# Performance work log

Hardware: AMD Instinct MI355X
Metric: run time of the kernel (lower is better)

The kernel has to match this reference:

```python
import jax, jax.numpy as jnp
import numpy as np

EMBED_DIM = 512
NUM_HEADS = 8
N_WIRES = 8  # kernel uses only first N_WIRES dims of each head vector


def setup_inputs() -> dict:
    key = jax.random.key(0)
    x = jax.random.normal(key, (8, 1024, EMBED_DIM), dtype=jnp.float32)
    return {"x": x}


def reference(x):
    B, S, E = x.shape
    H = NUM_HEADS
    dk = E // H
    # [B, H, S, dk]
    xh = x.reshape(B, S, H, dk).transpose(0, 2, 1, 3)
    # Quantum RY-overlap kernel closed form:
    #   RY(-y) RY(x) |0> = RY(x - y) |0>  =>  <0...0|psi> = prod_w cos((x_w - y_w)/2)
    # Only the first N_WIRES components of each head vector are used
    # (states.view(-1)[0] reads the first batch row's |0..0> amplitude).
    xw = xh[..., :N_WIRES]  # [B, H, S, NW]
    scores = jnp.ones((B, H, S, S), dtype=x.dtype)
    for w in range(N_WIRES):  # fixed small loop, fuses under jit
        diff = xw[:, :, :, None, w] - xw[:, :, None, :, w]  # [B, H, S, S]
        scores = scores * jnp.cos(diff * 0.5)
    scores = jnp.abs(scores)
    attn = jax.nn.softmax(scores, axis=-1)  # dropout is identity at eval
    out = jnp.einsum("bhij,bhjd->bhid", attn, xh)  # [B, H, S, dk]
    return out.transpose(0, 2, 1, 3).reshape(B, S, E)
```

## Files before the change

kernel.cpp:

```cpp
#include <hip/hip_runtime.h>

#define B_  8
#define S_  1024
#define E_  512
#define TI  64
#define TJ  64

typedef _Float16 half_t;
typedef _Float16 half2_t __attribute__((ext_vector_type(2)));
typedef _Float16 half8_t __attribute__((ext_vector_type(8)));
typedef float    floatx16 __attribute__((ext_vector_type(16)));
typedef unsigned int uint2v __attribute__((ext_vector_type(2)));
typedef unsigned int uint4v __attribute__((ext_vector_type(4)));

#define PHI_BYTES ((size_t)64 * S_ * 32 * 2)
#define VT_BYTES  ((size_t)64 * 64 * S_ * 2)

#define GLOAD_LDS16(g, l)                                                        \
    __builtin_amdgcn_global_load_lds((const __attribute__((address_space(1))) void*)(g), \
                                     (__attribute__((address_space(3))) void*)(l), 16, 0, 0)

__global__ __launch_bounds__(256) void precompute_kernel(const float* __restrict__ x,
                                                         half_t* __restrict__ phi,
                                                         half_t* __restrict__ vt) {
    const int bh  = blockIdx.y;
    const int b   = bh >> 3, h = bh & 7;
    const int jb0 = blockIdx.x * 128;
    const int t   = threadIdx.x;
    __shared__ half_t tsh[128 * 65];

    {
        const int jj = t >> 1, sel = t & 1;
        const int j  = jb0 + jj;
        const float* px = x + (size_t)b * S_ * E_ + (size_t)j * E_ + h * 64 + sel * 4;
        float4 w = *(const float4*)px;
        float xi[4] = {w.x, w.y, w.z, w.w};
        float c[4], s[4];
        #pragma unroll
        for (int q = 0; q < 4; ++q) {
            float v = xi[q] * 0.5f;
            c[q] = __cosf(v); s[q] = __sinf(v);
        }
        float pa[4] = {c[0]*c[1], s[0]*c[1], c[0]*s[1], s[0]*s[1]};
        float pb[4] = {c[2]*c[3], s[2]*c[3], c[2]*s[3], s[2]*s[3]};
        half_t f16[16];
        #pragma unroll
        for (int f = 0; f < 16; ++f)
            f16[f] = (half_t)(pa[f & 3] * pb[f >> 2]);
        half_t* dst = phi + ((size_t)bh * S_ + j) * 32 + (sel ? 0 : 16);
        *(half8_t*)dst       = *(half8_t*)&f16[0];
        *(half8_t*)(dst + 8) = *(half8_t*)&f16[8];
    }

    {
        const float* xb = x + (size_t)b * S_ * E_ + h * 64;
        for (int k = 0; k < 32; ++k) {
            int idx = k * 256 + t;
            int j = idx >> 6, d = idx & 63;
            tsh[j * 65 + d] = (half_t)xb[(size_t)(jb0 + j) * E_ + d];
        }
        __syncthreads();
        for (int k = 0; k < 32; ++k) {
            int idx = k * 256 + t;
            int d = idx >> 7, j = idx & 127;
            vt[((size_t)bh * 64 + d) * S_ + jb0 + j] = tsh[j * 65 + d];
        }
    }
}

__global__ __launch_bounds__(256, 4) void attn_kernel(const half_t* __restrict__ phi,
                                                      const half_t* __restrict__ vt,
                                                      float* __restrict__ out) {
    const int iblk = blockIdx.x;
    const int bh   = blockIdx.y;
    const int b    = bh >> 3, h = bh & 7;
    const int i0   = iblk * TI;
    const int t    = threadIdx.x;
    const int wv   = t >> 6, ln = t & 63;
    const int m    = ln & 31, hf = ln >> 5;
    const int ib   = wv >> 1, jb = wv & 1;

    __shared__ __align__(16) half_t sh_v[8 * 64 * 8];
    __shared__ float sh_red[2][32][64];
    __shared__ float sh_den[2][64];

    const half_t* phb = phi + (size_t)bh * S_ * 32;

    half8_t biH, biL;
    {
        const half_t* pr = phb + (size_t)(i0 + ib * 32 + m) * 32 + hf * 8;
        biH = *(const half8_t*)pr;
        biL = *(const half8_t*)(pr + 16);
    }

    floatx16 acc0, acc1, z;
    #pragma unroll
    for (int k = 0; k < 16; ++k) { acc0[k] = 0.f; acc1[k] = 0.f; z[k] = 0.f; }
    float d0 = 0.f, d1 = 0.f;

    const half_t* vsrc = vt + ((size_t)bh * 64 + ln) * S_;
    const half_t* asrc = phb + (size_t)(jb * 32 + m) * 32 + hf * 8;

    for (int j0 = 0; j0 < S_; j0 += TJ) {
        __syncthreads();

        GLOAD_LDS16(vsrc + j0 + (2 * wv + 0) * 8, &sh_v[(2 * wv + 0) * 64 * 8]);
        GLOAD_LDS16(vsrc + j0 + (2 * wv + 1) * 8, &sh_v[(2 * wv + 1) * 64 * 8]);

        const half_t* ar = asrc + (size_t)j0 * 32;
        half8_t ajH = *(const half8_t*)ar;
        half8_t ajL = *(const half8_t*)(ar + 16);

        floatx16 sH = __builtin_amdgcn_mfma_f32_32x32x16_f16(ajH, biH, z, 0, 0, 0);
        floatx16 sL = __builtin_amdgcn_mfma_f32_32x32x16_f16(ajL, biL, z, 0, 0, 0);

        unsigned int dwa[4], dwb[4];
        #pragma unroll
        for (int g = 0; g < 4; ++g) {
            float p[4];
            #pragma unroll
            for (int r = 0; r < 4; ++r) {
                float sc = sH[4 * g + r] * sL[4 * g + r];
                p[r] = __expf(__builtin_fabsf(sc));
            }
            d0 += p[0] + p[2];
            d1 += p[1] + p[3];
            half2_t ha = {(half_t)p[0], (half_t)p[1]};
            half2_t hb = {(half_t)p[2], (half_t)p[3]};
            dwa[g] = __builtin_bit_cast(unsigned int, ha);
            dwb[g] = __builtin_bit_cast(unsigned int, hb);
        }
        uint2v swA0 = __builtin_amdgcn_permlane32_swap(dwa[0], dwa[1], false, false);
        uint2v swB0 = __builtin_amdgcn_permlane32_swap(dwb[0], dwb[1], false, false);
        uint2v swA1 = __builtin_amdgcn_permlane32_swap(dwa[2], dwa[3], false, false);
        uint2v swB1 = __builtin_amdgcn_permlane32_swap(dwb[2], dwb[3], false, false);
        half8_t ap0 = __builtin_bit_cast(half8_t, (uint4v){swA0.x, swB0.x, swA0.y, swB0.y});
        half8_t ap1 = __builtin_bit_cast(half8_t, (uint4v){swA1.x, swB1.x, swA1.y, swB1.y});

        __syncthreads();

        const int q0 = jb * 4;
        half8_t b00 = *(const half8_t*)&sh_v[(((q0 + 0 + hf) * 64) + m) * 8];
        half8_t b01 = *(const half8_t*)&sh_v[(((q0 + 2 + hf) * 64) + m) * 8];
        half8_t b10 = *(const half8_t*)&sh_v[(((q0 + 0 + hf) * 64) + 32 + m) * 8];
        half8_t b11 = *(const half8_t*)&sh_v[(((q0 + 2 + hf) * 64) + 32 + m) * 8];

        acc0 = __builtin_amdgcn_mfma_f32_32x32x16_f16(ap0, b00, acc0, 0, 0, 0);
        acc0 = __builtin_amdgcn_mfma_f32_32x32x16_f16(ap1, b01, acc0, 0, 0, 0);
        acc1 = __builtin_amdgcn_mfma_f32_32x32x16_f16(ap0, b10, acc1, 0, 0, 0);
        acc1 = __builtin_amdgcn_mfma_f32_32x32x16_f16(ap1, b11, acc1, 0, 0, 0);
    }

    float dtot = d0 + d1;
    dtot += __shfl_xor(dtot, 32, 64);
    sh_den[jb][ib * 32 + m] = dtot;
    if (jb == 1) {
        #pragma unroll
        for (int reg = 0; reg < 16; ++reg) {
            int il = (reg & 3) + 8 * (reg >> 2) + 4 * hf;
            sh_red[ib][il][m]      = acc0[reg];
            sh_red[ib][il][32 + m] = acc1[reg];
        }
    }
    __syncthreads();
    if (jb == 0) {
        #pragma unroll
        for (int reg = 0; reg < 16; ++reg) {
            int il = (reg & 3) + 8 * (reg >> 2) + 4 * hf;
            float inv = 1.f / (sh_den[0][ib * 32 + il] + sh_den[1][ib * 32 + il]);
            size_t base = ((size_t)(b * S_ + i0 + ib * 32 + il)) * E_ + h * 64 + m;
            out[base]      = (acc0[reg] + sh_red[ib][il][m])      * inv;
            out[base + 32] = (acc1[reg] + sh_red[ib][il][32 + m]) * inv;
        }
    }
}

extern "C" void kernel_launch(void* const* d_in, const int* in_sizes, int n_in,
                              void* d_out, int out_size, void* d_ws, size_t ws_size,
                              hipStream_t stream) {
    const float* x = (const float*)d_in[0];
    float* out = (float*)d_out;
    half_t* phi = (half_t*)d_ws;
    half_t* vt  = (half_t*)((char*)d_ws + PHI_BYTES);
    precompute_kernel<<<dim3(8, 64), 256, 0, stream>>>(x, phi, vt);
    attn_kernel<<<dim3(S_ / TI, 64), 256, 0, stream>>>(phi, vt, out);
}
```

Measured before the change: 106.2 us.

## Double-buffer V tiles, prefetch phi rows, fold log2e into phi for exp2

The attention loop now double-buffers the V tile in LDS and prefetches the next phi-A fragment. This overlaps the global-to-LDS loads with the MFMA and exp work and leaves one barrier per iteration instead of two. The log2(e) factor is folded into one half of the j-side phi features, so the inner loop can use a raw exp2 instead of __expf. The precompute kernel stages x through LDS with vectorized loads and stores for the transpose, and writes a second scaled phi copy. The extra phi buffer adds workspace and write traffic, and scaling in half precision adds a small rounding change.

```diff
diff --git a/kernel.cpp b/kernel.cpp
--- a/kernel.cpp
+++ b/kernel.cpp
@@ -5,6 +5,7 @@
 #define E_  512
 #define TI  64
 #define TJ  64
+#define LOG2E 1.44269504088896340736f
 
 typedef _Float16 half_t;
 typedef _Float16 half2_t __attribute__((ext_vector_type(2)));
@@ -20,21 +21,31 @@
     __builtin_amdgcn_global_load_lds((const __attribute__((address_space(1))) void*)(g), \
                                      (__attribute__((address_space(3))) void*)(l), 16, 0, 0)
 
-__global__ __launch_bounds__(256) void precompute_kernel(const float* __restrict__ x,
-                                                         half_t* __restrict__ phi,
-                                                         half_t* __restrict__ vt) {
-    const int bh  = blockIdx.y;
-    const int b   = bh >> 3, h = bh & 7;
-    const int jb0 = blockIdx.x * 128;
-    const int t   = threadIdx.x;
-    __shared__ half_t tsh[128 * 65];
+__global__ __launch_bounds__(256, 4) void precompute_kernel(const float* __restrict__ x,
+                                                            half_t* __restrict__ phiA,
+                                                            half_t* __restrict__ phiB,
+                                                            half_t* __restrict__ vt) {
+    const int bh = blockIdx.y;
+    const int b  = bh >> 3, h = bh & 7;
+    const int j0 = blockIdx.x * 64;
+    const int t  = threadIdx.x;
+    __shared__ __align__(16) float vf[64][76];
+
+    const float* xb = x + (size_t)b * S_ * E_ + h * 64;
 
     {
+        const int j = t >> 2, dq = (t & 3) * 4;
+        const float* row = xb + (size_t)(j0 + j) * E_;
+        #pragma unroll
+        for (int q = 0; q < 4; ++q)
+            *(float4*)&vf[j][dq + q * 16] = *(const float4*)(row + dq + q * 16);
+    }
+    __syncthreads();
+
+    if (t < 128) {
         const int jj = t >> 1, sel = t & 1;
-        const int j  = jb0 + jj;
-        const float* px = x + (size_t)b * S_ * E_ + (size_t)j * E_ + h * 64 + sel * 4;
-        float4 w = *(const float4*)px;
-        float xi[4] = {w.x, w.y, w.z, w.w};
+        float4 xw = *(const float4*)&vf[jj][sel * 4];
+        float xi[4] = {xw.x, xw.y, xw.z, xw.w};
         float c[4], s[4];
         #pragma unroll
         for (int q = 0; q < 4; ++q) {
@@ -43,32 +54,34 @@
         }
         float pa[4] = {c[0]*c[1], s[0]*c[1], c[0]*s[1], s[0]*s[1]};
         float pb[4] = {c[2]*c[3], s[2]*c[3], c[2]*s[3], s[2]*s[3]};
-        half_t f16[16];
-        #pragma unroll
-        for (int f = 0; f < 16; ++f)
-            f16[f] = (half_t)(pa[f & 3] * pb[f >> 2]);
-        half_t* dst = phi + ((size_t)bh * S_ + j) * 32 + (sel ? 0 : 16);
-        *(half8_t*)dst       = *(half8_t*)&f16[0];
-        *(half8_t*)(dst + 8) = *(half8_t*)&f16[8];
+        const float scale = sel ? LOG2E : 1.0f;
+        half_t hB[16], hA[16];
+        #pragma unroll
+        for (int f = 0; f < 16; ++f) {
+            float v = pa[f & 3] * pb[f >> 2];
+            hB[f] = (half_t)v;
+            hA[f] = (half_t)(v * scale);
+        }
+        size_t off = ((size_t)bh * S_ + j0 + jj) * 32 + (sel ? 0 : 16);
+        *(half8_t*)(phiB + off)     = *(half8_t*)&hB[0];
+        *(half8_t*)(phiB + off + 8) = *(half8_t*)&hB[8];
+        *(half8_t*)(phiA + off)     = *(half8_t*)&hA[0];
+        *(half8_t*)(phiA + off + 8) = *(half8_t*)&hA[8];
     }
 
     {
-        const float* xb = x + (size_t)b * S_ * E_ + h * 64;
-        for (int k = 0; k < 32; ++k) {
-            int idx = k * 256 + t;
-            int j = idx >> 6, d = idx & 63;
-            tsh[j * 65 + d] = (half_t)xb[(size_t)(jb0 + j) * E_ + d];
-        }
-        __syncthreads();
-        for (int k = 0; k < 32; ++k) {
-            int idx = k * 256 + t;
-            int d = idx >> 7, j = idx & 127;
-            vt[((size_t)bh * 64 + d) * S_ + jb0 + j] = tsh[j * 65 + d];
-        }
+        const int d = t >> 2, jg = (t & 3) * 16;
+        half_t hv[16];
+        #pragma unroll
+        for (int k = 0; k < 16; ++k) hv[k] = (half_t)vf[jg + k][d];
+        half_t* dst = vt + ((size_t)bh * 64 + d) * S_ + j0 + jg;
+        *(half8_t*)dst       = *(half8_t*)&hv[0];
+        *(half8_t*)(dst + 8) = *(half8_t*)&hv[8];
     }
 }
 
-__global__ __launch_bounds__(256, 4) void attn_kernel(const half_t* __restrict__ phi,
+__global__ __launch_bounds__(256, 4) void attn_kernel(const half_t* __restrict__ phiA,
+                                                      const half_t* __restrict__ phiB,
                                                       const half_t* __restrict__ vt,
                                                       float* __restrict__ out) {
     const int iblk = blockIdx.x;
@@ -80,15 +93,16 @@
     const int m    = ln & 31, hf = ln >> 5;
     const int ib   = wv >> 1, jb = wv & 1;
 
-    __shared__ __align__(16) half_t sh_v[8 * 64 * 8];
+    __shared__ __align__(16) half_t sh_v[2][8 * 64 * 8];
     __shared__ float sh_red[2][32][64];
     __shared__ float sh_den[2][64];
 
-    const half_t* phb = phi + (size_t)bh * S_ * 32;
+    const half_t* phbA = phiA + (size_t)bh * S_ * 32;
+    const half_t* phbB = phiB + (size_t)bh * S_ * 32;
 
     half8_t biH, biL;
     {
-        const half_t* pr = phb + (size_t)(i0 + ib * 32 + m) * 32 + hf * 8;
+        const half_t* pr = phbB + (size_t)(i0 + ib * 32 + m) * 32 + hf * 8;
         biH = *(const half8_t*)pr;
         biL = *(const half8_t*)(pr + 16);
     }
@@ -99,17 +113,40 @@
     float d0 = 0.f, d1 = 0.f;
 
     const half_t* vsrc = vt + ((size_t)bh * 64 + ln) * S_;
-    const half_t* asrc = phb + (size_t)(jb * 32 + m) * 32 + hf * 8;
-
-    for (int j0 = 0; j0 < S_; j0 += TJ) {
-        __syncthreads();
-
-        GLOAD_LDS16(vsrc + j0 + (2 * wv + 0) * 8, &sh_v[(2 * wv + 0) * 64 * 8]);
-        GLOAD_LDS16(vsrc + j0 + (2 * wv + 1) * 8, &sh_v[(2 * wv + 1) * 64 * 8]);
-
-        const half_t* ar = asrc + (size_t)j0 * 32;
-        half8_t ajH = *(const half8_t*)ar;
-        half8_t ajL = *(const half8_t*)(ar + 16);
+    const half_t* asrc = phbA + (size_t)(jb * 32 + m) * 32 + hf * 8;
+
+    GLOAD_LDS16(vsrc + (2 * wv + 0) * 8, &sh_v[0][(2 * wv + 0) * 64 * 8]);
+    GLOAD_LDS16(vsrc + (2 * wv + 1) * 8, &sh_v[0][(2 * wv + 1) * 64 * 8]);
+    __builtin_amdgcn_sched_barrier(0);
+    half8_t ajH = *(const half8_t*)(asrc);
+    half8_t ajL = *(const half8_t*)(asrc + 16);
+    asm volatile("s_waitcnt vmcnt(2)" ::: "memory");
+    __builtin_amdgcn_s_barrier();
+
+    #pragma unroll
+    for (int tt = 0; tt < 16; ++tt) {
+        const int cur = tt & 1;
+        const int j0  = tt * TJ;
+
+        if (tt < 15) {
+            GLOAD_LDS16(vsrc + (j0 + TJ) + (2 * wv + 0) * 8, &sh_v[cur ^ 1][(2 * wv + 0) * 64 * 8]);
+            GLOAD_LDS16(vsrc + (j0 + TJ) + (2 * wv + 1) * 8, &sh_v[cur ^ 1][(2 * wv + 1) * 64 * 8]);
+        }
+        __builtin_amdgcn_sched_barrier(0);
+
+        const half_t* vb = sh_v[cur];
+        const int q0 = jb * 4;
+        half8_t b00 = *(const half8_t*)&vb[(((q0 + 0 + hf) * 64) + m) * 8];
+        half8_t b01 = *(const half8_t*)&vb[(((q0 + 2 + hf) * 64) + m) * 8];
+        half8_t b10 = *(const half8_t*)&vb[(((q0 + 0 + hf) * 64) + 32 + m) * 8];
+        half8_t b11 = *(const half8_t*)&vb[(((q0 + 2 + hf) * 64) + 32 + m) * 8];
+
+        half8_t ajHn, ajLn;
+        if (tt < 15) {
+            const half_t* ar = asrc + (size_t)(j0 + TJ) * 32;
+            ajHn = *(const half8_t*)ar;
+            ajLn = *(const half8_t*)(ar + 16);
+        } else { ajHn = ajH; ajLn = ajL; }
 
         floatx16 sH = __builtin_amdgcn_mfma_f32_32x32x16_f16(ajH, biH, z, 0, 0, 0);
         floatx16 sL = __builtin_amdgcn_mfma_f32_32x32x16_f16(ajL, biL, z, 0, 0, 0);
@@ -121,7 +158,7 @@
             #pragma unroll
             for (int r = 0; r < 4; ++r) {
                 float sc = sH[4 * g + r] * sL[4 * g + r];
-                p[r] = __expf(__builtin_fabsf(sc));
+                p[r] = __builtin_amdgcn_exp2f(__builtin_fabsf(sc));
             }
             d0 += p[0] + p[2];
             d1 += p[1] + p[3];
@@ -137,18 +174,14 @@
         half8_t ap0 = __builtin_bit_cast(half8_t, (uint4v){swA0.x, swB0.x, swA0.y, swB0.y});
         half8_t ap1 = __builtin_bit_cast(half8_t, (uint4v){swA1.x, swB1.x, swA1.y, swB1.y});
 
-        __syncthreads();
-
-        const int q0 = jb * 4;
-        half8_t b00 = *(const half8_t*)&sh_v[(((q0 + 0 + hf) * 64) + m) * 8];
-        half8_t b01 = *(const half8_t*)&sh_v[(((q0 + 2 + hf) * 64) + m) * 8];
-        half8_t b10 = *(const half8_t*)&sh_v[(((q0 + 0 + hf) * 64) + 32 + m) * 8];
-        half8_t b11 = *(const half8_t*)&sh_v[(((q0 + 2 + hf) * 64) + 32 + m) * 8];
-
         acc0 = __builtin_amdgcn_mfma_f32_32x32x16_f16(ap0, b00, acc0, 0, 0, 0);
         acc0 = __builtin_amdgcn_mfma_f32_32x32x16_f16(ap1, b01, acc0, 0, 0, 0);
         acc1 = __builtin_amdgcn_mfma_f32_32x32x16_f16(ap0, b10, acc1, 0, 0, 0);
         acc1 = __builtin_amdgcn_mfma_f32_32x32x16_f16(ap1, b11, acc1, 0, 0, 0);
+
+        if (tt < 15) { asm volatile("s_waitcnt vmcnt(2)" ::: "memory"); }
+        __builtin_amdgcn_s_barrier();
+        ajH = ajHn; ajL = ajLn;
     }
 
     float dtot = d0 + d1;
@@ -180,8 +213,9 @@
                               hipStream_t stream) {
     const float* x = (const float*)d_in[0];
     float* out = (float*)d_out;
-    half_t* phi = (half_t*)d_ws;
-    half_t* vt  = (half_t*)((char*)d_ws + PHI_BYTES);
-    precompute_kernel<<<dim3(8, 64), 256, 0, stream>>>(x, phi, vt);
-    attn_kernel<<<dim3(S_ / TI, 64), 256, 0, stream>>>(phi, vt, out);
+    half_t* phiA = (half_t*)d_ws;
+    half_t* phiB = (half_t*)((char*)d_ws + PHI_BYTES);
+    half_t* vt   = (half_t*)((char*)d_ws + 2 * PHI_BYTES);
+    precompute_kernel<<<dim3(16, 64), 256, 0, stream>>>(x, phiA, phiB, vt);
+    attn_kernel<<<dim3(S_ / TI, 64), 256, 0, stream>>>(phiA, phiB, vt, out);
 }
```

Result: slower. 177.5 us (+67.1%).
